# Kernel optimization log

Measured on AMD Instinct MI355X. Metric: run time of the kernel, lower is better.

## Reference

```python
import jax, jax.numpy as jnp
import numpy as np

B, GS, IN, HID = 256, 32, 512, 1024
HW = GS * GS

def setup_inputs() -> dict:
    key = jax.random.key(0)
    ks = jax.random.split(key, 18)
    s = 0.02
    return {
        "grid": jax.random.normal(ks[0], (B, 1, GS, GS), jnp.float32),
        "conv1_w": jax.random.normal(ks[1], (8, 1, 3, 3), jnp.float32) * s,
        "conv1_b": jax.random.normal(ks[2], (8,), jnp.float32) * s,
        "conv2_w": jax.random.normal(ks[3], (16, 8, 3, 3), jnp.float32) * s,
        "conv2_b": jax.random.normal(ks[4], (16,), jnp.float32) * s,
        "lin_w": jax.random.normal(ks[5], (IN, HW * 16), jnp.float32) * s,
        "lin_b": jax.random.normal(ks[6], (IN,), jnp.float32) * s,
        "gru_wih": jax.random.normal(ks[7], (3 * HID, IN + HW + 1), jnp.float32) * s,
        "gru_whh": jax.random.normal(ks[8], (3 * HID, HID), jnp.float32) * s,
        "gru_bih": jax.random.normal(ks[9], (3 * HID,), jnp.float32) * s,
        "gru_bhh": jax.random.normal(ks[10], (3 * HID,), jnp.float32) * s,
        "write_w": jax.random.normal(ks[11], (HW, HID), jnp.float32) * s,
        "write_b": jax.random.normal(ks[12], (HW,), jnp.float32) * s,
        "inc_w": jax.random.normal(ks[13], (1, HID), jnp.float32) * s,
        "inc_b": jax.random.normal(ks[14], (1,), jnp.float32) * s,
        "term_w": jax.random.normal(ks[15], (1, HID), jnp.float32) * s,
        "term_b": jax.random.normal(ks[16], (1,), jnp.float32) * s,
        "max_steps": 100,
    }

def _conv(x, w, b):
    y = jax.lax.conv_general_dilated(x, w, (1, 1), "SAME",
                                     dimension_numbers=("NCHW", "OIHW", "NCHW"))
    return y + b[None, :, None, None]

def _gru_cell(x, h, wih, whh, bih, bhh):
    gi = x @ wih.T + bih            # (B, 3H)
    gh = h @ whh.T + bhh
    ir, iz, inn = jnp.split(gi, 3, axis=1)
    hr, hz, hn = jnp.split(gh, 3, axis=1)
    r = jax.nn.sigmoid(ir + hr)
    z = jax.nn.sigmoid(iz + hz)
    n = jnp.tanh(inn + r * hn)
    return (1.0 - z) * n + z * h

def reference(grid, conv1_w, conv1_b, conv2_w, conv2_b, lin_w, lin_b,
              gru_wih, gru_whh, gru_bih, gru_bhh,
              write_w, write_b, inc_w, inc_b, term_w, term_b, max_steps):
    bsz = grid.shape[0]
    feat = jax.nn.relu(_conv(grid, conv1_w, conv1_b))
    feat = jax.nn.relu(_conv(feat, conv2_w, conv2_b))
    feat = feat.reshape(bsz, -1) @ lin_w.T + lin_b     # (B, IN), torch Flatten is channel-major

    def step(carry, _):
        h, mask, count, done = carry
        x = jnp.concatenate([feat, mask, count], axis=1)
        h2 = _gru_cell(x, h, gru_wih, gru_whh, gru_bih, gru_bhh)
        write = jax.nn.sigmoid(h2 @ write_w.T + write_b)
        inc = jax.nn.sigmoid(h2 @ inc_w.T + inc_b)
        term = jax.nn.sigmoid(h2 @ term_w.T + term_b)
        upd = jnp.logical_not(done)
        h_n = jnp.where(upd, h2, h)
        mask_n = jnp.where(upd, mask + write, mask)
        count_n = jnp.where(upd, count + inc, count)
        done_n = jnp.logical_or(done, jnp.all(term > 0.5))
        return (h_n, mask_n, count_n, done_n), None

    init = (jnp.zeros((bsz, HID), grid.dtype),
            jnp.zeros((bsz, HW), grid.dtype),
            jnp.zeros((bsz, 1), grid.dtype),
            jnp.array(False))
    (h, mask, count, done), _ = jax.lax.scan(step, init, None, length=max_steps)
    return count, mask
```

## Files before the change

kernel.cpp:

```cpp
#include <hip/hip_runtime.h>
#include <hip/hip_cooperative_groups.h>

namespace cg = cooperative_groups;

#define DEVI static __device__ __forceinline__

typedef __attribute__((ext_vector_type(8))) short s8v;
typedef __attribute__((ext_vector_type(4))) float f32x4;
typedef unsigned short us_t;
typedef unsigned int u32;

constexpr int NT_ = 256;
constexpr int B_ = 256, HW_ = 1024, IN_ = 512, HID_ = 1024, H3_ = 3072;
constexpr int XD_ = 1537;
constexpr int FLAT_ = 16384;

constexpr int OFF_WIHFBF = 0;
constexpr int OFF_WIHM2  = 393216;
constexpr int OFF_WHHBF  = 3538944;
constexpr int OFF_WIHC   = 5111808;
constexpr int OFF_CNTD   = 5114880;
constexpr int OFF_FLAGS  = 5115136;
constexpr int OFF_FEATBF = 5115264;
constexpr int OFF_GI     = 5180800;
constexpr int OFF_GH     = 5967232;
constexpr int OFF_H0     = 6753664;
constexpr int OFF_H1     = 7015808;
constexpr int OFF_WSIG   = 7277952;
constexpr int OFF_HHI    = 7540096;
constexpr int OFF_WSIG2  = 7671168;
constexpr int OFF_C2BF   = 7933312;
constexpr int OFF_LINWBF = 10030464;
constexpr int OFF_PART = OFF_GI;
constexpr int OFF_PW   = OFF_C2BF;
constexpr int OFF_PA2  = 14224768;
constexpr int OFF_WWBF = 20516224;

struct Params {
  const float* grid;
  const float* c1w; const float* c1b;
  const float* c2w; const float* c2b;
  const float* linw; const float* linb;
  const float* wih; const float* whh;
  const float* bih; const float* bhh;
  const float* ww;  const float* wb;
  const float* incw; const float* incb;
  const float* termw; const float* termb;
  const int* max_steps;
  float* out;
  float* ws;
};

DEVI float sigm(float x) { return 1.f / (1.f + __expf(-x)); }
DEVI float tanh_(float x) { return 1.f - 2.f / (__expf(2.f * x) + 1.f); }
DEVI float2 ld2(const float* p) { return *(const float2*)p; }
DEVI void ld4(float* d, const float* p) {
  float4 v = *(const float4*)p; d[0] = v.x; d[1] = v.y; d[2] = v.z; d[3] = v.w;
}
DEVI us_t f2bf(float x) {
  union { float f; u32 u; } v; v.f = x;
  u32 r = v.u + 0x7FFFu + ((v.u >> 16) & 1u);
  return (us_t)(r >> 16);
}
DEVI float bf2f(us_t h) {
  union { u32 u; float f; } v; v.u = ((u32)h) << 16; return v.f;
}
DEVI u32 pack2(float a, float b) { return (u32)f2bf(a) | ((u32)f2bf(b) << 16); }

__global__ __launch_bounds__(NT_) void conv_kernel(Params p) {
  __shared__ float s_in[20 * 34];
  __shared__ float s_c1[8 * 18 * 34];
  const int tid = threadIdx.x;
  const int b = blockIdx.x >> 1;
  const int r0 = (blockIdx.x & 1) * 16;
  for (int i = tid; i < 20 * 34; i += NT_) s_in[i] = 0.f;
  for (int i = tid; i < 8 * 18 * 34; i += NT_) s_c1[i] = 0.f;
  __syncthreads();
  for (int i = tid; i < 20 * 32; i += NT_) {
    const int ry = i >> 5, x = i & 31;
    const int iy = r0 - 2 + ry;
    if (iy >= 0 && iy < 32)
      s_in[ry * 34 + x + 1] = p.grid[b * 1024 + iy * 32 + x];
  }
  __syncthreads();
  if (tid < 144) {
    const int cy = tid >> 3;
    const int xg = (tid & 7) * 4;
    const int cr = r0 - 1 + cy;
    if (cr >= 0 && cr < 32) {
      float win[3][6];
      #pragma unroll
      for (int dy = 0; dy < 3; ++dy)
        #pragma unroll
        for (int c = 0; c < 6; ++c) win[dy][c] = s_in[(cy + dy) * 34 + xg + c];
      float acc[8][4];
      #pragma unroll
      for (int oc = 0; oc < 8; ++oc)
        #pragma unroll
        for (int i = 0; i < 4; ++i) acc[oc][i] = p.c1b[oc];
      #pragma unroll
      for (int oc = 0; oc < 8; ++oc)
        #pragma unroll
        for (int dy = 0; dy < 3; ++dy)
          #pragma unroll
          for (int dx = 0; dx < 3; ++dx) {
            const float w = p.c1w[oc * 9 + dy * 3 + dx];
            #pragma unroll
            for (int i = 0; i < 4; ++i)
              acc[oc][i] = fmaf(w, win[dy][i + dx], acc[oc][i]);
          }
      #pragma unroll
      for (int oc = 0; oc < 8; ++oc)
        #pragma unroll
        for (int i = 0; i < 4; ++i)
          s_c1[oc * 612 + cy * 34 + xg + i + 1] = fmaxf(acc[oc][i], 0.f);
    }
  }
  __syncthreads();
  {
    const int pos = tid * 2;
    const int y2 = pos >> 5, x2 = pos & 31;
    float acc[16][2];
    #pragma unroll
    for (int oc = 0; oc < 16; ++oc) { acc[oc][0] = p.c2b[oc]; acc[oc][1] = p.c2b[oc]; }
    for (int ic = 0; ic < 8; ++ic) {
      float win[3][4];
      #pragma unroll
      for (int dy = 0; dy < 3; ++dy)
        #pragma unroll
        for (int c = 0; c < 4; ++c)
          win[dy][c] = s_c1[ic * 612 + (y2 + dy) * 34 + x2 + c];
      #pragma unroll
      for (int oc = 0; oc < 16; ++oc)
        #pragma unroll
        for (int dy = 0; dy < 3; ++dy)
          #pragma unroll
          for (int dx = 0; dx < 3; ++dx) {
            const float w = p.c2w[oc * 72 + ic * 9 + dy * 3 + dx];
            acc[oc][0] = fmaf(w, win[dy][dx + 0], acc[oc][0]);
            acc[oc][1] = fmaf(w, win[dy][dx + 1], acc[oc][1]);
          }
    }
    us_t* dst = (us_t*)(p.ws + OFF_C2BF) + b * FLAT_;
    #pragma unroll
    for (int oc = 0; oc < 16; ++oc)
      *(u32*)(dst + oc * 1024 + (r0 + y2) * 32 + x2) =
          pack2(fmaxf(acc[oc][0], 0.f), fmaxf(acc[oc][1], 0.f));
  }
}

__global__ __launch_bounds__(NT_) void prep_kernel(Params p) {
  const int gt = blockIdx.x * NT_ + threadIdx.x;
  const int gs = 2048 * NT_;
  us_t* wihf = (us_t*)(p.ws + OFF_WIHFBF);
  us_t* wihm2 = (us_t*)(p.ws + OFF_WIHM2);
  us_t* whhbf = (us_t*)(p.ws + OFF_WHHBF);
  us_t* linwbf = (us_t*)(p.ws + OFF_LINWBF);
  us_t* wwbf = (us_t*)(p.ws + OFF_WWBF);
  float* wihc = p.ws + OFF_WIHC;
  int* flags = (int*)(p.ws + OFF_FLAGS);
  for (int i = gt; i < (IN_ * FLAT_) / 4; i += gs) {
    float4 v = *(const float4*)(p.linw + (size_t)i * 4);
    *(uint2*)(linwbf + (size_t)i * 4) = make_uint2(pack2(v.x, v.y), pack2(v.z, v.w));
  }
  for (int i = gt; i < (H3_ * HID_) / 4; i += gs) {
    float4 v = *(const float4*)(p.whh + (size_t)i * 4);
    *(uint2*)(whhbf + (size_t)i * 4) = make_uint2(pack2(v.x, v.y), pack2(v.z, v.w));
  }
  for (int i = gt; i < (HID_ * HID_) / 4; i += gs) {
    float4 v = *(const float4*)(p.ww + (size_t)i * 4);
    *(uint2*)(wwbf + (size_t)i * 4) = make_uint2(pack2(v.x, v.y), pack2(v.z, v.w));
  }
  for (int i4 = gt; i4 < (H3_ * XD_) / 4; i4 += gs) {
    float4 v = *(const float4*)(p.wih + (size_t)i4 * 4);
    const float vv[4] = {v.x, v.y, v.z, v.w};
    #pragma unroll
    for (int e = 0; e < 4; ++e) {
      const int i = i4 * 4 + e;
      const int n = i / XD_;
      const int k = i - n * XD_;
      const float x = vv[e];
      if (k < 512) {
        wihf[n * 512 + k] = f2bf(x);
      } else if (k < 1536) {
        const int kk = k - 512;
        const us_t hi = f2bf(x);
        wihm2[(size_t)n * 2048 + kk] = hi;
        wihm2[(size_t)n * 2048 + 1024 + kk] = f2bf(x - bf2f(hi));
      } else {
        wihc[n] = x;
      }
    }
  }
  if (gt < 128) flags[gt] = 1;
}

DEVI void mfma_block(const us_t* __restrict__ Ag, int lda,
                     const us_t* __restrict__ Bg, int ldb, int nc,
                     us_t* __restrict__ sA, us_t* __restrict__ sB,
                     float* __restrict__ dst, int ldd) {
  const int tid = threadIdx.x;
  const int ar = tid >> 3, au = tid & 7;
  const int sw = au ^ (ar & 7);
  const int abase = (ar * 8 + sw) * 8;
  const us_t* a0p = Ag + (size_t)ar * lda + au * 8;
  const us_t* a1p = Ag + (size_t)(ar + 32) * lda + au * 8;
  const us_t* b0p = Bg + (size_t)ar * ldb + au * 8;
  const us_t* b1p = b0p + (size_t)32 * ldb;
  const us_t* b2p = b0p + (size_t)64 * ldb;
  const us_t* b3p = b0p + (size_t)96 * ldb;
  f32x4 acc[4][2];
  #pragma unroll
  for (int f = 0; f < 4; ++f) { acc[f][0] = (f32x4)0.f; acc[f][1] = (f32x4)0.f; }
  s8v ra0 = *(const s8v*)a0p;
  s8v ra1 = *(const s8v*)a1p;
  s8v rb0 = *(const s8v*)b0p;
  s8v rb1 = *(const s8v*)b1p;
  s8v rb2 = *(const s8v*)b2p;
  s8v rb3 = *(const s8v*)b3p;
  const int w = tid >> 6;
  const int lane = tid & 63;
  const int l15 = lane & 15, l4 = lane >> 4;
  const int rsw = l15 & 7;
  int c = 0;
  for (;;) {
    __syncthreads();
    *(s8v*)(sA + abase) = ra0;
    *(s8v*)(sA + abase + 2048) = ra1;
    *(s8v*)(sB + abase) = rb0;
    *(s8v*)(sB + abase + 2048) = rb1;
    *(s8v*)(sB + abase + 4096) = rb2;
    *(s8v*)(sB + abase + 6144) = rb3;
    ++c;
    if (c < nc) {
      const int ko = c * 64;
      ra0 = *(const s8v*)(a0p + ko);
      ra1 = *(const s8v*)(a1p + ko);
      rb0 = *(const s8v*)(b0p + ko);
      rb1 = *(const s8v*)(b1p + ko);
      rb2 = *(const s8v*)(b2p + ko);
      rb3 = *(const s8v*)(b3p + ko);
    }
    __syncthreads();
    #pragma unroll
    for (int kk = 0; kk < 2; ++kk) {
      const int uoff = ((kk * 4 + l4) ^ rsw) * 8;
      s8v bA = *(const s8v*)(sB + (w * 32 + l15) * 64 + uoff);
      s8v bB = *(const s8v*)(sB + (w * 32 + 16 + l15) * 64 + uoff);
      #pragma unroll
      for (int f = 0; f < 4; ++f) {
        s8v a = *(const s8v*)(sA + (f * 16 + l15) * 64 + uoff);
        acc[f][0] = __builtin_amdgcn_mfma_f32_16x16x32_bf16(a, bA, acc[f][0], 0, 0, 0);
        acc[f][1] = __builtin_amdgcn_mfma_f32_16x16x32_bf16(a, bB, acc[f][1], 0, 0, 0);
      }
    }
    if (c >= nc) break;
  }
  #pragma unroll
  for (int f = 0; f < 4; ++f)
    #pragma unroll
    for (int g = 0; g < 2; ++g) {
      float* dp = dst + (size_t)(f * 16 + l4 * 4) * ldd + w * 32 + g * 16 + l15;
      #pragma unroll
      for (int j = 0; j < 4; ++j) dp[(size_t)j * ldd] = acc[f][g][j];
    }
}

__global__ __launch_bounds__(NT_) void lin_mfma(Params p) {
  __shared__ us_t sm[12288];
  const int b = blockIdx.x;
  const int ks = b & 15, t = b >> 4;
  const int mt = t >> 2, nt = t & 3;
  const us_t* A = (us_t*)(p.ws + OFF_C2BF) + (size_t)mt * 64 * FLAT_ + ks * 1024;
  const us_t* B = (us_t*)(p.ws + OFF_LINWBF) + (size_t)nt * 128 * FLAT_ + ks * 1024;
  float* dst = p.ws + OFF_PART + ks * (B_ * IN_) + mt * 64 * IN_ + nt * 128;
  mfma_block(A, FLAT_, B, FLAT_, 16, sm, sm + 4096, dst, IN_);
}

__global__ __launch_bounds__(NT_) void red_kernel(Params p) {
  const int gt = blockIdx.x * NT_ + threadIdx.x;
  const int o = gt & (IN_ - 1);
  const float* part = p.ws + OFF_PART;
  float s = p.linb[o];
  #pragma unroll
  for (int ks = 0; ks < 16; ++ks) s += part[ks * (B_ * IN_) + gt];
  ((us_t*)(p.ws + OFF_FEATBF))[gt] = f2bf(s);
}

__global__ __launch_bounds__(NT_) void a1_mfma(Params p) {
  __shared__ us_t sm[12288];
  const int b = blockIdx.x;
  const int mt = b / 24, nt = b - mt * 24;
  const us_t* A = (us_t*)(p.ws + OFF_FEATBF) + (size_t)mt * 64 * IN_;
  const us_t* B = (us_t*)(p.ws + OFF_WIHFBF) + (size_t)nt * 128 * IN_;
  float* dst = p.ws + OFF_GI + (size_t)mt * 64 * H3_ + nt * 128;
  mfma_block(A, IN_, B, IN_, 8, sm, sm + 4096, dst, H3_);
}

__global__ __launch_bounds__(NT_) void stepA_mfma(Params p, int step) {
  if (((volatile int*)(p.ws + OFF_FLAGS))[step - 1]) return;
  __shared__ us_t sm[12288];
  const int b = blockIdx.x;
  if (b < 576) {
    const int term = b / 192;
    const int r = b - term * 192;
    const int ks = r / 96;
    const int t = r - ks * 96;
    const int mt = t / 24, nt = t - mt * 24;
    const us_t* A = (us_t*)(p.ws + OFF_WSIG2) + (size_t)mt * 64 * 2048 +
                    (term == 1 ? 1024 : 0) + ks * 512;
    const us_t* B = (us_t*)(p.ws + OFF_WIHM2) + (size_t)nt * 128 * 2048 +
                    (term == 2 ? 1024 : 0) + ks * 512;
    float* dst = p.ws + OFF_PA2 + (size_t)(term * 2 + ks) * 786432 +
                 (size_t)mt * 64 * H3_ + nt * 128;
    mfma_block(A, 2048, B, 2048, 8, sm, sm + 4096, dst, H3_);
  } else {
    const int r = b - 576;
    const int ks = r / 96;
    const int t = r - ks * 96;
    const int mt = t / 24, nt = t - mt * 24;
    const us_t* A = (us_t*)(p.ws + OFF_HHI) + (size_t)mt * 64 * HID_ + ks * 512;
    const us_t* B = (us_t*)(p.ws + OFF_WHHBF) + (size_t)nt * 128 * HID_ + ks * 512;
    float* dst = p.ws + OFF_PA2 + (size_t)(6 + ks) * 786432 +
                 (size_t)mt * 64 * H3_ + nt * 128;
    mfma_block(A, HID_, B, HID_, 8, sm, sm + 4096, dst, H3_);
  }
}

__global__ __launch_bounds__(NT_) void stepG_kernel(Params p, int step) {
  int* flags = (int*)(p.ws + OFF_FLAGS);
  if (step > 0 && ((volatile int*)flags)[step - 1]) return;
  __shared__ float sred[8];
  const int row = blockIdx.x;
  const int tid = threadIdx.x;
  const size_t base = (size_t)row * H3_;
  float* const gi = p.ws + OFF_GI + base;
  const float* const pA = p.ws + OFF_PA2;
  const float* const wihc = p.ws + OFF_WIHC;
  const float* hold = p.ws + ((step & 1) ? OFF_H1 : OFF_H0) + (size_t)row * HID_;
  float* hnew = p.ws + ((step & 1) ? OFF_H0 : OFF_H1) + (size_t)row * HID_;
  us_t* hhi = (us_t*)(p.ws + OFF_HHI) + (size_t)row * HID_;
  const float cd = (step > 0) ? (p.ws + OFF_CNTD)[row] : 0.f;
  float incd = 0.f, termd = 0.f;
  #pragma unroll
  for (int q = 0; q < 4; ++q) {
    const int c = tid + q * NT_;
    float gr_ = gi[c], gz_ = gi[1024 + c], gn_ = gi[2048 + c];
    float hr_ = 0.f, hz_ = 0.f, hn_ = 0.f, hv = 0.f;
    if (step > 0) {
      #pragma unroll
      for (int t6 = 0; t6 < 6; ++t6) {
        const float* pp = pA + (size_t)t6 * 786432 + base;
        gr_ += pp[c]; gz_ += pp[1024 + c]; gn_ += pp[2048 + c];
      }
      gr_ += cd * wihc[c];
      gz_ += cd * wihc[1024 + c];
      gn_ += cd * wihc[2048 + c];
      const float* q6 = pA + (size_t)6 * 786432 + base;
      const float* q7 = pA + (size_t)7 * 786432 + base;
      hr_ = q6[c] + q7[c];
      hz_ = q6[1024 + c] + q7[1024 + c];
      hn_ = q6[2048 + c] + q7[2048 + c];
      gi[c] = gr_; gi[1024 + c] = gz_; gi[2048 + c] = gn_;
      hv = hold[c];
    }
    float rr = sigm(gr_ + p.bih[c] + hr_ + p.bhh[c]);
    float zz = sigm(gz_ + p.bih[1024 + c] + hz_ + p.bhh[1024 + c]);
    float nn = tanh_(gn_ + p.bih[2048 + c] + rr * (hn_ + p.bhh[2048 + c]));
    float h2 = (1.f - zz) * nn + zz * hv;
    hnew[c] = h2;
    hhi[c] = f2bf(h2);
    incd = fmaf(h2, p.incw[c], incd);
    termd = fmaf(h2, p.termw[c], termd);
  }
  #pragma unroll
  for (int off = 32; off > 0; off >>= 1) {
    incd += __shfl_down(incd, off);
    termd += __shfl_down(termd, off);
  }
  if ((tid & 63) == 0) { sred[tid >> 6] = incd; sred[4 + (tid >> 6)] = termd; }
  __syncthreads();
  if (tid == 0) {
    float it = sred[0] + sred[1] + sred[2] + sred[3];
    float tt = sred[4] + sred[5] + sred[6] + sred[7];
    float cdn = sigm(it + p.incb[0]);
    (p.ws + OFF_CNTD)[row] = cdn;
    if (step == 0) p.out[row] = cdn;
    else p.out[row] += cdn;
    if (tt + p.termb[0] <= 0.f) atomicAnd(&flags[step], 0);
  }
}

__global__ __launch_bounds__(NT_) void stepW_mfma(Params p, int step) {
  if (step > 0 && ((volatile int*)(p.ws + OFF_FLAGS))[step - 1]) return;
  __shared__ us_t sm[12288];
  const int b = blockIdx.x;
  const int ks = b & 7, t = b >> 3;
  const int mt = t >> 3, nt = t & 7;
  const us_t* A = (us_t*)(p.ws + OFF_HHI) + (size_t)mt * 64 * HID_ + ks * 128;
  const us_t* B = (us_t*)(p.ws + OFF_WWBF) + (size_t)nt * 128 * HID_ + ks * 128;
  float* dst = p.ws + OFF_PW + ks * (B_ * HW_) + (size_t)mt * 64 * HW_ + nt * 128;
  mfma_block(A, HID_, B, HID_, 2, sm, sm + 4096, dst, HW_);
}

__global__ __launch_bounds__(NT_) void stepWepi_kernel(Params p, int step) {
  if (step > 0 && ((volatile int*)(p.ws + OFF_FLAGS))[step - 1]) return;
  const int i = (blockIdx.x * NT_ + threadIdx.x) * 4;
  const int m = i >> 10, n = i & 1023;
  const float* pW = p.ws + OFF_PW;
  float4 s = *(const float4*)(p.wb + n);
  #pragma unroll
  for (int ks = 0; ks < 8; ++ks) {
    float4 v = *(const float4*)(pW + ks * (B_ * HW_) + i);
    s.x += v.x; s.y += v.y; s.z += v.z; s.w += v.w;
  }
  float4 sv = {sigm(s.x), sigm(s.y), sigm(s.z), sigm(s.w)};
  float* op = p.out + B_ + i;
  if (step == 0) {
    *(float4*)op = sv;
  } else {
    float4 ov = *(float4*)op;
    ov.x += sv.x; ov.y += sv.y; ov.z += sv.z; ov.w += sv.w;
    *(float4*)op = ov;
  }
  *(float4*)(p.ws + OFF_WSIG + i) = sv;
  us_t* w2 = (us_t*)(p.ws + OFF_WSIG2) + (size_t)m * 2048 + n;
  us_t h0 = f2bf(sv.x), h1 = f2bf(sv.y), h2b = f2bf(sv.z), h3 = f2bf(sv.w);
  *(uint2*)w2 = make_uint2((u32)h0 | ((u32)h1 << 16), (u32)h2b | ((u32)h3 << 16));
  *(uint2*)(w2 + 1024) = make_uint2(
      pack2(sv.x - bf2f(h0), sv.y - bf2f(h1)),
      pack2(sv.z - bf2f(h2b), sv.w - bf2f(h3)));
}

DEVI void b_job(const Params& p, float* sh2, float* swb,
                const float* gi, const float* gh, const float* hold,
                float* hnew, float* wsig, float* cntd, int* dflag, int job) {
  const int tid = threadIdx.x;
  const int mt = job >> 3, nt = job & 7;
  const int r0 = mt * 8, c0 = nt * 128;
  const int gr = tid >> 5;
  const int gk = (tid & 31) * 2;
  const int wr = tid & 7;
  const int wc = (tid >> 3) * 4;
  const int row = r0 + gr;
  const float* giR = gi + row * H3_;
  const float* ghR = gh + row * H3_;
  const float* hR = hold + row * HID_;
  float* hW = hnew + row * HID_;
  float acc[4] = {0.f, 0.f, 0.f, 0.f};
  float incd = 0.f, termd = 0.f;
  const bool wh = (nt == 0);
  for (int kc = 0; kc < HID_; kc += 64) {
    float2 gxr = ld2(giR + kc + gk);
    float2 gxz = ld2(giR + 1024 + kc + gk);
    float2 gxn = ld2(giR + 2048 + kc + gk);
    float2 ghr = ld2(ghR + kc + gk);
    float2 ghz = ld2(ghR + 1024 + kc + gk);
    float2 ghn = ld2(ghR + 2048 + kc + gk);
    float2 hol = ld2(hR + kc + gk);
    float2 bri = ld2(p.bih + kc + gk);
    float2 brh = ld2(p.bhh + kc + gk);
    float2 bzi = ld2(p.bih + 1024 + kc + gk);
    float2 bzh = ld2(p.bhh + 1024 + kc + gk);
    float2 bni = ld2(p.bih + 2048 + kc + gk);
    float2 bnh = ld2(p.bhh + 2048 + kc + gk);
    float2 iw = ld2(p.incw + kc + gk);
    float2 tw = ld2(p.termw + kc + gk);
    float h2[2];
    {
      float rr = sigm(gxr.x + bri.x + ghr.x + brh.x);
      float zz = sigm(gxz.x + bzi.x + ghz.x + bzh.x);
      float nn = tanh_(gxn.x + bni.x + rr * (ghn.x + bnh.x));
      h2[0] = (1.f - zz) * nn + zz * hol.x;
      rr = sigm(gxr.y + bri.y + ghr.y + brh.y);
      zz = sigm(gxz.y + bzi.y + ghz.y + bzh.y);
      nn = tanh_(gxn.y + bni.y + rr * (ghn.y + bnh.y));
      h2[1] = (1.f - zz) * nn + zz * hol.y;
    }
    incd = fmaf(h2[0], iw.x, fmaf(h2[1], iw.y, incd));
    termd = fmaf(h2[0], tw.x, fmaf(h2[1], tw.y, termd));
    float4 wreg[8];
    #pragma unroll
    for (int it = 0; it < 8; ++it) {
      int id = tid + it * 256;
      int c = id >> 4, k4 = (id & 15) * 4;
      wreg[it] = *(const float4*)(p.ww + (c0 + c) * HID_ + kc + k4);
    }
    __syncthreads();
    sh2[gr * 68 + gk] = h2[0];
    sh2[gr * 68 + gk + 1] = h2[1];
    #pragma unroll
    for (int it = 0; it < 8; ++it) {
      int id = tid + it * 256;
      int c = id >> 4, k4 = (id & 15) * 4;
      swb[(k4 + 0) * 132 + c] = wreg[it].x;
      swb[(k4 + 1) * 132 + c] = wreg[it].y;
      swb[(k4 + 2) * 132 + c] = wreg[it].z;
      swb[(k4 + 3) * 132 + c] = wreg[it].w;
    }
    if (wh) {
      *(float2*)(hW + kc + gk) = make_float2(h2[0], h2[1]);
      *(u32*)((us_t*)(p.ws + OFF_HHI) + row * HID_ + kc + gk) = pack2(h2[0], h2[1]);
    }
    __syncthreads();
    #pragma unroll 8
    for (int kk = 0; kk < 64; ++kk) {
      float a = sh2[wr * 68 + kk];
      float4 b = *(const float4*)(swb + kk * 132 + wc);
      acc[0] = fmaf(a, b.x, acc[0]);
      acc[1] = fmaf(a, b.y, acc[1]);
      acc[2] = fmaf(a, b.z, acc[2]);
      acc[3] = fmaf(a, b.w, acc[3]);
    }
  }
  if (wh) {
    #pragma unroll
    for (int off = 16; off > 0; off >>= 1) {
      incd += __shfl_down(incd, off, 32);
      termd += __shfl_down(termd, off, 32);
    }
    if ((tid & 31) == 0) {
      float cd = sigm(incd + p.incb[0]);
      cntd[row] = cd;
      p.out[row] += cd;
      if (termd + p.termb[0] <= 0.f) atomicAnd(dflag, 0);
    }
  }
  {
    const int m = r0 + wr;
    float4 wb4 = *(const float4*)(p.wb + c0 + wc);
    float4 sv = {sigm(acc[0] + wb4.x), sigm(acc[1] + wb4.y),
                 sigm(acc[2] + wb4.z), sigm(acc[3] + wb4.w)};
    float* op = p.out + B_ + m * HW_ + c0 + wc;
    float4 ov = *(float4*)op;
    ov.x += sv.x; ov.y += sv.y; ov.z += sv.z; ov.w += sv.w;
    *(float4*)op = ov;
    *(float4*)(wsig + m * HID_ + c0 + wc) = sv;
    us_t* w2 = (us_t*)(p.ws + OFF_WSIG2) + m * 2048 + c0 + wc;
    us_t h0 = f2bf(sv.x), h1 = f2bf(sv.y), h2b = f2bf(sv.z), h3 = f2bf(sv.w);
    *(uint2*)w2 = make_uint2((u32)h0 | ((u32)h1 << 16), (u32)h2b | ((u32)h3 << 16));
    *(uint2*)(w2 + 1024) = make_uint2(
        pack2(sv.x - bf2f(h0), sv.y - bf2f(h1)),
        pack2(sv.z - bf2f(h2b), sv.w - bf2f(h3)));
  }
}

template <bool SB>
DEVI void gemm_db64(const float* __restrict__ A, int lda,
                    const float* __restrict__ Bw, int ldb, int K,
                    float* __restrict__ As, float* __restrict__ Bs,
                    float (&acc)[4][4]) {
  constexpr int P = 68;
  const int tid = threadIdx.x;
  const int tx = tid & 15, ty = tid >> 4;
  const int lr = tid >> 2, lk = (tid & 3) << 2;
  #pragma unroll
  for (int i = 0; i < 4; ++i)
    #pragma unroll
    for (int j = 0; j < 4; ++j) acc[i][j] = 0.f;
  auto ldb4 = [&](int k0) {
    float4 v;
    if constexpr (SB) {
      const float* q = Bw + (size_t)lr * ldb + k0 + lk;
      v.x = q[0]; v.y = q[1]; v.z = q[2]; v.w = q[3];
    } else {
      v = *(const float4*)(Bw + (size_t)lr * ldb + k0 + lk);
    }
    return v;
  };
  float4 va = *(const float4*)(A + lr * lda + lk);
  float4 vb = ldb4(0);
  As[(lk + 0) * P + lr] = va.x; As[(lk + 1) * P + lr] = va.y;
  As[(lk + 2) * P + lr] = va.z; As[(lk + 3) * P + lr] = va.w;
  Bs[(lk + 0) * P + lr] = vb.x; Bs[(lk + 1) * P + lr] = vb.y;
  Bs[(lk + 2) * P + lr] = vb.z; Bs[(lk + 3) * P + lr] = vb.w;
  __syncthreads();
  int cur = 0;
  for (int k0 = 16; k0 < K; k0 += 16) {
    va = *(const float4*)(A + lr * lda + k0 + lk);
    vb = ldb4(k0);
    const float* as = As + cur * (16 * P);
    const float* bs = Bs + cur * (16 * P);
    #pragma unroll
    for (int kk = 0; kk < 16; ++kk) {
      float a[4], b[4];
      ld4(a, as + kk * P + ty * 4);
      ld4(b, bs + kk * P + tx * 4);
      #pragma unroll
      for (int i = 0; i < 4; ++i)
        #pragma unroll
        for (int j = 0; j < 4; ++j) acc[i][j] = fmaf(a[i], b[j], acc[i][j]);
    }
    __syncthreads();
    float* asw = As + (cur ^ 1) * (16 * P);
    float* bsw = Bs + (cur ^ 1) * (16 * P);
    asw[(lk + 0) * P + lr] = va.x; asw[(lk + 1) * P + lr] = va.y;
    asw[(lk + 2) * P + lr] = va.z; asw[(lk + 3) * P + lr] = va.w;
    bsw[(lk + 0) * P + lr] = vb.x; bsw[(lk + 1) * P + lr] = vb.y;
    bsw[(lk + 2) * P + lr] = vb.z; bsw[(lk + 3) * P + lr] = vb.w;
    __syncthreads();
    cur ^= 1;
  }
  const float* as = As + cur * (16 * P);
  const float* bs = Bs + cur * (16 * P);
  #pragma unroll
  for (int kk = 0; kk < 16; ++kk) {
    float a[4], b[4];
    ld4(a, as + kk * P + ty * 4);
    ld4(b, bs + kk * P + tx * 4);
    #pragma unroll
    for (int i = 0; i < 4; ++i)
      #pragma unroll
      for (int j = 0; j < 4; ++j) acc[i][j] = fmaf(a[i], b[j], acc[i][j]);
  }
}

__global__ __launch_bounds__(NT_, 2) void tail_kernel(Params p, int start) {
  int* flags = (int*)(p.ws + OFF_FLAGS);
  if (((volatile int*)flags)[start - 1]) return;
  cg::grid_group gg = cg::this_grid();
  __shared__ __align__(16) float smem[8992];
  float* As = smem;
  float* Bs = smem + 2176;
  float* sh2 = smem;
  float* swb = smem + 544;
  float* const ws = p.ws;
  float* const gi = ws + OFF_GI;
  float* const gh = ws + OFF_GH;
  float* const wsig = ws + OFF_WSIG;
  float* const cntd = ws + OFF_CNTD;
  const float* const wihc = ws + OFF_WIHC;
  const int tid = threadIdx.x;
  const int bid = blockIdx.x;
  const int nb = gridDim.x;
  const int tx = tid & 15, ty = tid >> 4;
  const int msteps = p.max_steps[0];

  for (int step = start; step < msteps; ++step) {
    float* hcur = ws + ((step & 1) ? OFF_H1 : OFF_H0);
    float* hnxt = ws + ((step & 1) ? OFF_H0 : OFF_H1);
    for (int job = bid; job < 384; job += nb) {
      float acc[4][4];
      if (job < 192) {
        const int mt = job / 48, nt = job - mt * 48;
        gemm_db64<true>(wsig + mt * 64 * HID_, HID_,
                        p.wih + (size_t)nt * 64 * XD_ + 512, XD_, HID_, As, Bs, acc);
        #pragma unroll
        for (int i = 0; i < 4; ++i) {
          const int m = mt * 64 + ty * 4 + i;
          const float cd = cntd[m];
          float4 wc4 = *(const float4*)(wihc + nt * 64 + tx * 4);
          float* gp = gi + m * H3_ + nt * 64 + tx * 4;
          float4 g = *(float4*)gp;
          g.x += acc[i][0] + cd * wc4.x;
          g.y += acc[i][1] + cd * wc4.y;
          g.z += acc[i][2] + cd * wc4.z;
          g.w += acc[i][3] + cd * wc4.w;
          *(float4*)gp = g;
        }
      } else {
        const int j = job - 192;
        const int mt = j / 48, nt = j - mt * 48;
        gemm_db64<false>(hcur + mt * 64 * HID_, HID_,
                         p.whh + (size_t)nt * 64 * HID_, HID_, HID_, As, Bs, acc);
        #pragma unroll
        for (int i = 0; i < 4; ++i) {
          float4 v = {acc[i][0], acc[i][1], acc[i][2], acc[i][3]};
          *(float4*)(gh + (mt * 64 + ty * 4 + i) * H3_ + nt * 64 + tx * 4) = v;
        }
      }
      __syncthreads();
    }
    gg.sync();
    for (int job = bid; job < 256; job += nb)
      b_job(p, sh2, swb, gi, gh, hcur, hnxt, wsig, cntd, &flags[step], job);
    gg.sync();
    if (((volatile int*)flags)[step]) break;
  }
}

extern "C" void kernel_launch(void* const* d_in, const int* in_sizes, int n_in,
                              void* d_out, int out_size, void* d_ws, size_t ws_size,
                              hipStream_t stream) {
  (void)in_sizes; (void)n_in; (void)out_size; (void)ws_size;
  Params prm;
  prm.grid = (const float*)d_in[0];
  prm.c1w  = (const float*)d_in[1];
  prm.c1b  = (const float*)d_in[2];
  prm.c2w  = (const float*)d_in[3];
  prm.c2b  = (const float*)d_in[4];
  prm.linw = (const float*)d_in[5];
  prm.linb = (const float*)d_in[6];
  prm.wih  = (const float*)d_in[7];
  prm.whh  = (const float*)d_in[8];
  prm.bih  = (const float*)d_in[9];
  prm.bhh  = (const float*)d_in[10];
  prm.ww   = (const float*)d_in[11];
  prm.wb   = (const float*)d_in[12];
  prm.incw = (const float*)d_in[13];
  prm.incb = (const float*)d_in[14];
  prm.termw = (const float*)d_in[15];
  prm.termb = (const float*)d_in[16];
  prm.max_steps = (const int*)d_in[17];
  prm.out = (float*)d_out;
  prm.ws = (float*)d_ws;

  hipLaunchKernelGGL(conv_kernel, dim3(512), dim3(NT_), 0, stream, prm);
  hipLaunchKernelGGL(prep_kernel, dim3(2048), dim3(NT_), 0, stream, prm);
  hipLaunchKernelGGL(lin_mfma, dim3(256), dim3(NT_), 0, stream, prm);
  hipLaunchKernelGGL(red_kernel, dim3(512), dim3(NT_), 0, stream, prm);
  hipLaunchKernelGGL(a1_mfma, dim3(96), dim3(NT_), 0, stream, prm);

  constexpr int U = 2;
  hipLaunchKernelGGL(stepG_kernel, dim3(B_), dim3(NT_), 0, stream, prm, 0);
  hipLaunchKernelGGL(stepW_mfma, dim3(256), dim3(NT_), 0, stream, prm, 0);
  hipLaunchKernelGGL(stepWepi_kernel, dim3(256), dim3(NT_), 0, stream, prm, 0);
  for (int t = 1; t < U; ++t) {
    hipLaunchKernelGGL(stepA_mfma, dim3(768), dim3(NT_), 0, stream, prm, t);
    hipLaunchKernelGGL(stepG_kernel, dim3(B_), dim3(NT_), 0, stream, prm, t);
    hipLaunchKernelGGL(stepW_mfma, dim3(256), dim3(NT_), 0, stream, prm, t);
    hipLaunchKernelGGL(stepWepi_kernel, dim3(256), dim3(NT_), 0, stream, prm, t);
  }
  int start = U;
  void* args[] = {(void*)&prm, (void*)&start};
  (void)hipLaunchCooperativeKernel((const void*)tail_kernel, dim3(384), dim3(NT_),
                                   args, 0, stream);
}
```

Before: 142.5 us.

## Convert fp32 weights to bf16 on the fly inside MFMA loads, drop prep copies

```diff
diff --git a/kernel.cpp b/kernel.cpp
--- a/kernel.cpp
+++ b/kernel.cpp
@@ -17,7 +17,6 @@
 
 constexpr int OFF_WIHFBF = 0;
 constexpr int OFF_WIHM2  = 393216;
-constexpr int OFF_WHHBF  = 3538944;
 constexpr int OFF_WIHC   = 5111808;
 constexpr int OFF_CNTD   = 5114880;
 constexpr int OFF_FLAGS  = 5115136;
@@ -30,11 +29,9 @@
 constexpr int OFF_HHI    = 7540096;
 constexpr int OFF_WSIG2  = 7671168;
 constexpr int OFF_C2BF   = 7933312;
-constexpr int OFF_LINWBF = 10030464;
 constexpr int OFF_PART = OFF_GI;
 constexpr int OFF_PW   = OFF_C2BF;
 constexpr int OFF_PA2  = 14224768;
-constexpr int OFF_WWBF = 20516224;
 
 struct Params {
   const float* grid;
@@ -67,6 +64,16 @@
 }
 DEVI u32 pack2(float a, float b) { return (u32)f2bf(a) | ((u32)f2bf(b) << 16); }
 
+DEVI s8v ld8w(const us_t* p) { return *(const s8v*)p; }
+DEVI s8v ld8w(const float* p) {
+  float4 v0 = *(const float4*)p;
+  float4 v1 = *(const float4*)(p + 4);
+  union { u32 u[4]; s8v s; } r;
+  r.u[0] = pack2(v0.x, v0.y); r.u[1] = pack2(v0.z, v0.w);
+  r.u[2] = pack2(v1.x, v1.y); r.u[3] = pack2(v1.z, v1.w);
+  return r.s;
+}
+
 __global__ __launch_bounds__(NT_) void conv_kernel(Params p) {
   __shared__ float s_in[20 * 34];
   __shared__ float s_c1[8 * 18 * 34];
@@ -151,26 +158,11 @@
 
 __global__ __launch_bounds__(NT_) void prep_kernel(Params p) {
   const int gt = blockIdx.x * NT_ + threadIdx.x;
-  const int gs = 2048 * NT_;
+  const int gs = 1024 * NT_;
   us_t* wihf = (us_t*)(p.ws + OFF_WIHFBF);
   us_t* wihm2 = (us_t*)(p.ws + OFF_WIHM2);
-  us_t* whhbf = (us_t*)(p.ws + OFF_WHHBF);
-  us_t* linwbf = (us_t*)(p.ws + OFF_LINWBF);
-  us_t* wwbf = (us_t*)(p.ws + OFF_WWBF);
   float* wihc = p.ws + OFF_WIHC;
   int* flags = (int*)(p.ws + OFF_FLAGS);
-  for (int i = gt; i < (IN_ * FLAT_) / 4; i += gs) {
-    float4 v = *(const float4*)(p.linw + (size_t)i * 4);
-    *(uint2*)(linwbf + (size_t)i * 4) = make_uint2(pack2(v.x, v.y), pack2(v.z, v.w));
-  }
-  for (int i = gt; i < (H3_ * HID_) / 4; i += gs) {
-    float4 v = *(const float4*)(p.whh + (size_t)i * 4);
-    *(uint2*)(whhbf + (size_t)i * 4) = make_uint2(pack2(v.x, v.y), pack2(v.z, v.w));
-  }
-  for (int i = gt; i < (HID_ * HID_) / 4; i += gs) {
-    float4 v = *(const float4*)(p.ww + (size_t)i * 4);
-    *(uint2*)(wwbf + (size_t)i * 4) = make_uint2(pack2(v.x, v.y), pack2(v.z, v.w));
-  }
   for (int i4 = gt; i4 < (H3_ * XD_) / 4; i4 += gs) {
     float4 v = *(const float4*)(p.wih + (size_t)i4 * 4);
     const float vv[4] = {v.x, v.y, v.z, v.w};
@@ -195,8 +187,9 @@
   if (gt < 128) flags[gt] = 1;
 }
 
+template <typename TB>
 DEVI void mfma_block(const us_t* __restrict__ Ag, int lda,
-                     const us_t* __restrict__ Bg, int ldb, int nc,
+                     const TB* __restrict__ Bg, int ldb, int nc,
                      us_t* __restrict__ sA, us_t* __restrict__ sB,
                      float* __restrict__ dst, int ldd) {
   const int tid = threadIdx.x;
@@ -205,19 +198,19 @@
   const int abase = (ar * 8 + sw) * 8;
   const us_t* a0p = Ag + (size_t)ar * lda + au * 8;
   const us_t* a1p = Ag + (size_t)(ar + 32) * lda + au * 8;
-  const us_t* b0p = Bg + (size_t)ar * ldb + au * 8;
-  const us_t* b1p = b0p + (size_t)32 * ldb;
-  const us_t* b2p = b0p + (size_t)64 * ldb;
-  const us_t* b3p = b0p + (size_t)96 * ldb;
+  const TB* b0p = Bg + (size_t)ar * ldb + au * 8;
+  const TB* b1p = Bg + (size_t)(ar + 32) * ldb + au * 8;
+  const TB* b2p = Bg + (size_t)(ar + 64) * ldb + au * 8;
+  const TB* b3p = Bg + (size_t)(ar + 96) * ldb + au * 8;
   f32x4 acc[4][2];
   #pragma unroll
   for (int f = 0; f < 4; ++f) { acc[f][0] = (f32x4)0.f; acc[f][1] = (f32x4)0.f; }
-  s8v ra0 = *(const s8v*)a0p;
-  s8v ra1 = *(const s8v*)a1p;
-  s8v rb0 = *(const s8v*)b0p;
-  s8v rb1 = *(const s8v*)b1p;
-  s8v rb2 = *(const s8v*)b2p;
-  s8v rb3 = *(const s8v*)b3p;
+  s8v ra0 = ld8w(a0p);
+  s8v ra1 = ld8w(a1p);
+  s8v rb0 = ld8w(b0p);
+  s8v rb1 = ld8w(b1p);
+  s8v rb2 = ld8w(b2p);
+  s8v rb3 = ld8w(b3p);
   const int w = tid >> 6;
   const int lane = tid & 63;
   const int l15 = lane & 15, l4 = lane >> 4;
@@ -234,12 +227,12 @@
     ++c;
     if (c < nc) {
       const int ko = c * 64;
-      ra0 = *(const s8v*)(a0p + ko);
-      ra1 = *(const s8v*)(a1p + ko);
-      rb0 = *(const s8v*)(b0p + ko);
-      rb1 = *(const s8v*)(b1p + ko);
-      rb2 = *(const s8v*)(b2p + ko);
-      rb3 = *(const s8v*)(b3p + ko);
+      ra0 = ld8w(a0p + ko);
+      ra1 = ld8w(a1p + ko);
+      rb0 = ld8w(b0p + ko);
+      rb1 = ld8w(b1p + ko);
+      rb2 = ld8w(b2p + ko);
+      rb3 = ld8w(b3p + ko);
     }
     __syncthreads();
     #pragma unroll
@@ -272,7 +265,7 @@
   const int ks = b & 15, t = b >> 4;
   const int mt = t >> 2, nt = t & 3;
   const us_t* A = (us_t*)(p.ws + OFF_C2BF) + (size_t)mt * 64 * FLAT_ + ks * 1024;
-  const us_t* B = (us_t*)(p.ws + OFF_LINWBF) + (size_t)nt * 128 * FLAT_ + ks * 1024;
+  const float* B = p.linw + (size_t)nt * 128 * FLAT_ + ks * 1024;
   float* dst = p.ws + OFF_PART + ks * (B_ * IN_) + mt * 64 * IN_ + nt * 128;
   mfma_block(A, FLAT_, B, FLAT_, 16, sm, sm + 4096, dst, IN_);
 }
@@ -301,30 +294,18 @@
   if (((volatile int*)(p.ws + OFF_FLAGS))[step - 1]) return;
   __shared__ us_t sm[12288];
   const int b = blockIdx.x;
-  if (b < 576) {
-    const int term = b / 192;
-    const int r = b - term * 192;
-    const int ks = r / 96;
-    const int t = r - ks * 96;
-    const int mt = t / 24, nt = t - mt * 24;
-    const us_t* A = (us_t*)(p.ws + OFF_WSIG2) + (size_t)mt * 64 * 2048 +
-                    (term == 1 ? 1024 : 0) + ks * 512;
-    const us_t* B = (us_t*)(p.ws + OFF_WIHM2) + (size_t)nt * 128 * 2048 +
-                    (term == 2 ? 1024 : 0) + ks * 512;
-    float* dst = p.ws + OFF_PA2 + (size_t)(term * 2 + ks) * 786432 +
-                 (size_t)mt * 64 * H3_ + nt * 128;
-    mfma_block(A, 2048, B, 2048, 8, sm, sm + 4096, dst, H3_);
-  } else {
-    const int r = b - 576;
-    const int ks = r / 96;
-    const int t = r - ks * 96;
-    const int mt = t / 24, nt = t - mt * 24;
-    const us_t* A = (us_t*)(p.ws + OFF_HHI) + (size_t)mt * 64 * HID_ + ks * 512;
-    const us_t* B = (us_t*)(p.ws + OFF_WHHBF) + (size_t)nt * 128 * HID_ + ks * 512;
-    float* dst = p.ws + OFF_PA2 + (size_t)(6 + ks) * 786432 +
-                 (size_t)mt * 64 * H3_ + nt * 128;
-    mfma_block(A, HID_, B, HID_, 8, sm, sm + 4096, dst, H3_);
-  }
+  const int term = b / 192;
+  const int r = b - term * 192;
+  const int ks = r / 96;
+  const int t = r - ks * 96;
+  const int mt = t / 24, nt = t - mt * 24;
+  const us_t* A = (us_t*)(p.ws + OFF_WSIG2) + (size_t)mt * 64 * 2048 +
+                  (term == 1 ? 1024 : 0) + ks * 512;
+  const us_t* B = (us_t*)(p.ws + OFF_WIHM2) + (size_t)nt * 128 * 2048 +
+                  (term == 2 ? 1024 : 0) + ks * 512;
+  float* dst = p.ws + OFF_PA2 + (size_t)(term * 2 + ks) * 786432 +
+               (size_t)mt * 64 * H3_ + nt * 128;
+  mfma_block(A, 2048, B, 2048, 8, sm, sm + 4096, dst, H3_);
 }
 
 __global__ __launch_bounds__(NT_) void stepG_kernel(Params p, int step) {
@@ -335,6 +316,7 @@
   const int tid = threadIdx.x;
   const size_t base = (size_t)row * H3_;
   float* const gi = p.ws + OFF_GI + base;
+  const float* const gh = p.ws + OFF_GH + base;
   const float* const pA = p.ws + OFF_PA2;
   const float* const wihc = p.ws + OFF_WIHC;
   const float* hold = p.ws + ((step & 1) ? OFF_H1 : OFF_H0) + (size_t)row * HID_;
@@ -356,12 +338,8 @@
       gr_ += cd * wihc[c];
       gz_ += cd * wihc[1024 + c];
       gn_ += cd * wihc[2048 + c];
-      const float* q6 = pA + (size_t)6 * 786432 + base;
-      const float* q7 = pA + (size_t)7 * 786432 + base;
-      hr_ = q6[c] + q7[c];
-      hz_ = q6[1024 + c] + q7[1024 + c];
-      hn_ = q6[2048 + c] + q7[2048 + c];
       gi[c] = gr_; gi[1024 + c] = gz_; gi[2048 + c] = gn_;
+      hr_ = gh[c]; hz_ = gh[1024 + c]; hn_ = gh[2048 + c];
       hv = hold[c];
     }
     float rr = sigm(gr_ + p.bih[c] + hr_ + p.bhh[c]);
@@ -392,15 +370,26 @@
 }
 
 __global__ __launch_bounds__(NT_) void stepW_mfma(Params p, int step) {
-  if (step > 0 && ((volatile int*)(p.ws + OFF_FLAGS))[step - 1]) return;
   __shared__ us_t sm[12288];
+  int* flags = (int*)(p.ws + OFF_FLAGS);
   const int b = blockIdx.x;
-  const int ks = b & 7, t = b >> 3;
-  const int mt = t >> 3, nt = t & 7;
-  const us_t* A = (us_t*)(p.ws + OFF_HHI) + (size_t)mt * 64 * HID_ + ks * 128;
-  const us_t* B = (us_t*)(p.ws + OFF_WWBF) + (size_t)nt * 128 * HID_ + ks * 128;
-  float* dst = p.ws + OFF_PW + ks * (B_ * HW_) + (size_t)mt * 64 * HW_ + nt * 128;
-  mfma_block(A, HID_, B, HID_, 2, sm, sm + 4096, dst, HW_);
+  if (b < 256) {
+    if (step > 0 && ((volatile int*)flags)[step - 1]) return;
+    const int ks = b & 7, t = b >> 3;
+    const int mt = t >> 3, nt = t & 7;
+    const us_t* A = (us_t*)(p.ws + OFF_HHI) + (size_t)mt * 64 * HID_ + ks * 128;
+    const float* B = p.ww + (size_t)nt * 128 * HID_ + ks * 128;
+    float* dst = p.ws + OFF_PW + ks * (B_ * HW_) + (size_t)mt * 64 * HW_ + nt * 128;
+    mfma_block(A, HID_, B, HID_, 2, sm, sm + 4096, dst, HW_);
+  } else {
+    if (((volatile int*)flags)[step]) return;
+    const int r = b - 256;
+    const int mt = r / 24, nt = r - mt * 24;
+    const us_t* A = (us_t*)(p.ws + OFF_HHI) + (size_t)mt * 64 * HID_;
+    const float* B = p.whh + (size_t)nt * 128 * HID_;
+    float* dst = p.ws + OFF_GH + (size_t)mt * 64 * H3_ + nt * 128;
+    mfma_block(A, HID_, B, HID_, 16, sm, sm + 4096, dst, H3_);
+  }
 }
 
 __global__ __launch_bounds__(NT_) void stepWepi_kernel(Params p, int step) {
@@ -706,22 +695,20 @@
   prm.ws = (float*)d_ws;
 
   hipLaunchKernelGGL(conv_kernel, dim3(512), dim3(NT_), 0, stream, prm);
-  hipLaunchKernelGGL(prep_kernel, dim3(2048), dim3(NT_), 0, stream, prm);
   hipLaunchKernelGGL(lin_mfma, dim3(256), dim3(NT_), 0, stream, prm);
+  hipLaunchKernelGGL(prep_kernel, dim3(1024), dim3(NT_), 0, stream, prm);
   hipLaunchKernelGGL(red_kernel, dim3(512), dim3(NT_), 0, stream, prm);
   hipLaunchKernelGGL(a1_mfma, dim3(96), dim3(NT_), 0, stream, prm);
 
-  constexpr int U = 2;
   hipLaunchKernelGGL(stepG_kernel, dim3(B_), dim3(NT_), 0, stream, prm, 0);
-  hipLaunchKernelGGL(stepW_mfma, dim3(256), dim3(NT_), 0, stream, prm, 0);
+  hipLaunchKernelGGL(stepW_mfma, dim3(352), dim3(NT_), 0, stream, prm, 0);
   hipLaunchKernelGGL(stepWepi_kernel, dim3(256), dim3(NT_), 0, stream, prm, 0);
-  for (int t = 1; t < U; ++t) {
-    hipLaunchKernelGGL(stepA_mfma, dim3(768), dim3(NT_), 0, stream, prm, t);
-    hipLaunchKernelGGL(stepG_kernel, dim3(B_), dim3(NT_), 0, stream, prm, t);
-    hipLaunchKernelGGL(stepW_mfma, dim3(256), dim3(NT_), 0, stream, prm, t);
-    hipLaunchKernelGGL(stepWepi_kernel, dim3(256), dim3(NT_), 0, stream, prm, t);
-  }
-  int start = U;
+  hipLaunchKernelGGL(stepA_mfma, dim3(576), dim3(NT_), 0, stream, prm, 1);
+  hipLaunchKernelGGL(stepG_kernel, dim3(B_), dim3(NT_), 0, stream, prm, 1);
+  hipLaunchKernelGGL(stepW_mfma, dim3(352), dim3(NT_), 0, stream, prm, 1);
+  hipLaunchKernelGGL(stepWepi_kernel, dim3(256), dim3(NT_), 0, stream, prm, 1);
+
+  int start = 2;
   void* args[] = {(void*)&prm, (void*)&start};
   (void)hipLaunchCooperativeKernel((const void*)tail_kernel, dim3(384), dim3(NT_),
                                    args, 0, stream);
```

Result: slower. 178.1 us (+25.0%).
